# Kernel tuning notes

Measured on AMD Instinct MI355X. Metric: run time of the kernel, lower is better.

## Reference

```python
import jax, jax.numpy as jnp
import numpy as np

D = 768       # input embedding dim
H = 256       # hidden_dim
NH = 4        # num_heads
HD = H // NH  # head_dim = 64
M = 131072    # number of candidate LLM embeddings


def setup_inputs() -> dict:
    key = jax.random.key(0)
    ks = jax.random.split(key, 16)
    s = 0.02
    return {
        "user": jax.random.normal(ks[0], (D,), jnp.float32),
        "query": jax.random.normal(ks[1], (D,), jnp.float32),
        "llm": jax.random.normal(ks[2], (M, D), jnp.float32),
        # projection weights (torch Linear: y = x @ W.T + b)
        "Wu": jax.random.normal(ks[3], (H, D), jnp.float32) * s,
        "bu": jnp.zeros((H,), jnp.float32),
        "Wq": jax.random.normal(ks[4], (H, D), jnp.float32) * s,
        "bq": jnp.zeros((H,), jnp.float32),
        "Wl": jax.random.normal(ks[5], (H, D), jnp.float32) * s,
        "bl": jnp.zeros((H,), jnp.float32),
        # MultiheadAttention packed in-projection [3H, H] and bias [3H]
        "in_proj_w": jax.random.normal(ks[6], (3 * H, H), jnp.float32) * s,
        "in_proj_b": jnp.zeros((3 * H,), jnp.float32),
        "out_proj_w": jax.random.normal(ks[7], (H, H), jnp.float32) * s,
        "out_proj_b": jnp.zeros((H,), jnp.float32),
        # final scoring linear: [1, 2H]
        "Wo": jax.random.normal(ks[8], (1, 2 * H), jnp.float32) * s,
        "bo": jnp.zeros((1,), jnp.float32),
    }


def reference(user, query, llm, Wu, bu, Wq, bq, Wl, bl,
              in_proj_w, in_proj_b, out_proj_w, out_proj_b, Wo, bo):
    m = llm.shape[0]
    # input projections
    u = user @ Wu.T + bu            # [H]
    qv = query @ Wq.T + bq          # [H]
    l = llm @ Wl.T + bl             # [M, H]
    # context rows are identical for every candidate -> compute K/V once on [2, H]
    ctx = jnp.stack([u, qv], axis=0)                      # [2, H]
    Wq_a, Wk_a, Wv_a = jnp.split(in_proj_w, 3, axis=0)    # each [H, H]
    bq_a, bk_a, bv_a = jnp.split(in_proj_b, 3, axis=0)
    q = (l @ Wq_a.T + bq_a).reshape(m, NH, HD)            # [M, nh, hd] (seq_len=1)
    k = (ctx @ Wk_a.T + bk_a).reshape(2, NH, HD)          # [2, nh, hd]
    v = (ctx @ Wv_a.T + bv_a).reshape(2, NH, HD)
    scale = 1.0 / jnp.sqrt(jnp.asarray(HD, q.dtype))
    scores = jnp.einsum('mhd,khd->mhk', q, k) * scale     # [M, nh, 2]
    attn = jax.nn.softmax(scores, axis=-1)
    attended = jnp.einsum('mhk,khd->mhd', attn, v).reshape(m, H)
    attended = attended @ out_proj_w.T + out_proj_b       # [M, H]
    x = jnp.concatenate([attended, l], axis=-1)           # [M, 2H]
    # out = Sequential(ReLU, Dropout(eval=identity), Linear(2H, 1))
    logits = (jax.nn.relu(x) @ Wo.T + bo).squeeze(-1)     # [M]
    return logits
```

## Files before the change

kernel.cpp:

```cpp
#include <hip/hip_runtime.h>


typedef float f32x4 __attribute__((ext_vector_type(4)));
typedef __bf16 bf16x8 __attribute__((ext_vector_type(8)));

#define VMCNT(n) asm volatile("s_waitcnt vmcnt(" #n ")" ::: "memory")

__device__ __forceinline__ unsigned f2bf(float f) {
  unsigned u = __builtin_bit_cast(unsigned, f);
  u += 0x7fffu + ((u >> 16) & 1u);
  return u >> 16;
}

__device__ __forceinline__ void gl_lds16(const void* g, void* l) {
  __builtin_amdgcn_global_load_lds(
      (const __attribute__((address_space(1))) void*)g,
      (__attribute__((address_space(3))) void*)l, 16, 0, 0);
}

__global__ void prep_a(const float* __restrict__ user, const float* __restrict__ query,
                       const float* __restrict__ Wu, const float* __restrict__ bu,
                       const float* __restrict__ Wq, const float* __restrict__ bq,
                       float* __restrict__ wf) {
  const int og = threadIdx.x >> 5, ln = threadIdx.x & 31;
  const int o = blockIdx.x * 8 + og;
  const int isq = o >> 8, j = o & 255;
  const float* Wrow = (isq ? Wq : Wu) + (size_t)j * 768;
  const float* vec = isq ? query : user;
  float p = 0.f;
  #pragma unroll
  for (int i = 0; i < 24; ++i) { int d = ln * 24 + i; p = fmaf(Wrow[d], vec[d], p); }
  #pragma unroll
  for (int off = 16; off; off >>= 1) p += __shfl_xor(p, off);
  if (ln == 0) wf[o] = p + (isq ? bq[j] : bu[j]);
}

__global__ void prep_b(const float* __restrict__ ipw, const float* __restrict__ ipb,
                       float* __restrict__ wf) {
  const int og = threadIdx.x >> 5, ln = threadIdx.x & 31;
  const int o = blockIdx.x * 8 + og;
  const int kv = o >> 9, cc = (o >> 8) & 1, j = o & 255;
  const int row = 256 + kv * 256 + j;
  const float* Wrow = ipw + (size_t)row * 256;
  const float* ctx = wf + cc * 256;
  float p = 0.f;
  #pragma unroll
  for (int i = 0; i < 8; ++i) { int d = ln * 8 + i; p = fmaf(Wrow[d], ctx[d], p); }
  #pragma unroll
  for (int off = 16; off; off >>= 1) p += __shfl_xor(p, off);
  if (ln == 0) wf[512 + o] = p + ipb[row];
}

__global__ void prep_c(const float* __restrict__ ipw, const float* __restrict__ ipb,
                       const float* __restrict__ opw, const float* __restrict__ opb,
                       float* __restrict__ wf) {
  const int t = threadIdx.x, b = blockIdx.x;
  if (b < 4) {
    const int h = b;
    float acc = 0.f;
    for (int d = 0; d < 64; ++d) {
      float kd = wf[512 + h * 64 + d] - wf[768 + h * 64 + d];
      acc = fmaf(ipw[(size_t)(h * 64 + d) * 256 + t], kd, acc);
    }
    wf[1536 + h * 256 + t] = 0.125f * acc;
    if (t == 0) {
      float cs = 0.f;
      for (int d = 0; d < 64; ++d)
        cs = fmaf(ipb[h * 64 + d], wf[512 + h * 64 + d] - wf[768 + h * 64 + d], cs);
      wf[3840 + h] = 0.125f * cs;
    }
  } else {
    const float* oprow = opw + (size_t)t * 256;
    float bse = 0.f;
    for (int i = 0; i < 256; ++i) bse = fmaf(oprow[i], wf[1280 + i], bse);
    wf[2560 + t] = bse + opb[t];
    #pragma unroll
    for (int h = 0; h < 4; ++h) {
      float dl = 0.f;
      for (int d = 0; d < 64; ++d)
        dl = fmaf(oprow[h * 64 + d], wf[1024 + h * 64 + d] - wf[1280 + h * 64 + d], dl);
      wf[2816 + h * 256 + t] = dl;
    }
  }
}

__global__ void prep_w(const float* __restrict__ Wl, unsigned int* __restrict__ Bs4) {
  const int tid = blockIdx.x * 256 + threadIdx.x;
  const int lane = tid & 63;
  const int ntk = tid >> 6;
  const int kk = ntk >> 4, nt = ntk & 15;
  const int k = kk * 32 + (lane >> 4) * 8;
  const int j = nt * 16 + (lane & 15);
  const float* src = Wl + (size_t)j * 768 + k;
  uint4 pk;
  pk.x = f2bf(src[0]) | (f2bf(src[1]) << 16);
  pk.y = f2bf(src[2]) | (f2bf(src[3]) << 16);
  pk.z = f2bf(src[4]) | (f2bf(src[5]) << 16);
  pk.w = f2bf(src[6]) | (f2bf(src[7]) << 16);
  ((uint4*)Bs4)[tid] = pk;
}

__global__ __launch_bounds__(256, 3) void fused_main(
    const float* __restrict__ llm, const float* __restrict__ bl,
    const float* __restrict__ Wo, const float* __restrict__ bo,
    const float* __restrict__ wf, float* __restrict__ out) {

  __shared__ __align__(16) char smem[49152];
  __shared__ float csd_s[4];
  __shared__ float a_s[64][4];
  __shared__ float r2_s[64];
  __shared__ float p2_s[4][64];

  const int t = threadIdx.x;
  const int w = t >> 6, l = t & 63, g = l >> 4, c = l & 15;
  const int m0 = blockIdx.x * 64;
  const char* BsB = (const char*)(wf + 4096);

  auto stage = [&](int buf, int kk) {
    char* abase = smem + buf * 8192 + w * 1024;
    #pragma unroll
    for (int r = 0; r < 2; ++r) {
      const int chunk = r * 256 + w * 64 + l;
      const int row = chunk >> 3;
      const int cb = (chunk & 7) * 16;
      const int cl = cb ^ ((row & 7) << 4);
      const char* gp = (const char*)(llm + (size_t)(m0 + row) * 768 + kk * 32) + cl;
      gl_lds16(gp, abase + r * 4096);
    }
    char* bbase = smem + 16384 + buf * 16384 + w * 1024;
    const char* gb = BsB + (size_t)kk * 16384;
    #pragma unroll
    for (int r = 0; r < 4; ++r) {
      const int chunk = r * 256 + w * 64 + l;
      gl_lds16(gb + (size_t)chunk * 16, bbase + r * 4096);
    }
  };

  stage(0, 0);

  f32x4 acc[16] = {};
  const int row_l = w * 16 + c;
  const int sro = row_l * 128;
  const int sxor = (row_l & 7) << 4;

  for (int kk = 0; kk < 24; ++kk) {
    const int cur = kk & 1;
    if (kk < 23) { stage(cur ^ 1, kk + 1); VMCNT(6); }
    else         { VMCNT(0); }
    __builtin_amdgcn_s_barrier();

    const char* ab = smem + cur * 8192 + sro;
    const float4 fa = *(const float4*)(ab + ((g * 32) ^ sxor));
    const float4 fb = *(const float4*)(ab + ((g * 32 + 16) ^ sxor));
    uint4 pk;
    pk.x = f2bf(fa.x) | (f2bf(fa.y) << 16);
    pk.y = f2bf(fa.z) | (f2bf(fa.w) << 16);
    pk.z = f2bf(fb.x) | (f2bf(fb.y) << 16);
    pk.w = f2bf(fb.z) | (f2bf(fb.w) << 16);
    const bf16x8 afr = __builtin_bit_cast(bf16x8, pk);

    const char* bb = smem + 16384 + cur * 16384 + l * 16;
    #pragma unroll
    for (int nt = 0; nt < 16; ++nt) {
      const bf16x8 bfr = *(const bf16x8*)(bb + nt * 1024);
      acc[nt] = __builtin_amdgcn_mfma_f32_16x16x32_bf16(afr, bfr, acc[nt], 0, 0, 0);
    }
    __builtin_amdgcn_s_barrier();
  }

  float* wsd_s  = (float*)smem;
  float* delta_s = (float*)smem + 1024;
  float* base_s = (float*)smem + 2048;
  float* woa_s  = (float*)smem + 2304;
  float* wo2_s  = (float*)smem + 2560;
  float* bl_s   = (float*)smem + 2816;
  for (int i = t; i < 1024; i += 256) { wsd_s[i] = wf[1536 + i]; delta_s[i] = wf[2816 + i]; }
  base_s[t] = wf[2560 + t];
  woa_s[t] = Wo[t];
  wo2_s[t] = Wo[256 + t];
  bl_s[t] = bl[t];
  if (t < 4) csd_s[t] = wf[3840 + t];
  __syncthreads();

  float psd[4][4] = {};
  float pr2[4] = {};
  #pragma unroll
  for (int nt = 0; nt < 16; ++nt) {
    const int col = nt * 16 + c;
    const float w0 = wsd_s[col], w1 = wsd_s[256 + col], w2 = wsd_s[512 + col], w3 = wsd_s[768 + col];
    const float wo = wo2_s[col], bb2 = bl_s[col];
    #pragma unroll
    for (int j = 0; j < 4; ++j) {
      const float x = acc[nt][j] + bb2;
      psd[j][0] = fmaf(x, w0, psd[j][0]);
      psd[j][1] = fmaf(x, w1, psd[j][1]);
      psd[j][2] = fmaf(x, w2, psd[j][2]);
      psd[j][3] = fmaf(x, w3, psd[j][3]);
      pr2[j] = fmaf(fmaxf(x, 0.f), wo, pr2[j]);
    }
  }
  #pragma unroll
  for (int off = 8; off; off >>= 1) {
    #pragma unroll
    for (int j = 0; j < 4; ++j) {
      #pragma unroll
      for (int h = 0; h < 4; ++h) psd[j][h] += __shfl_xor(psd[j][h], off);
      pr2[j] += __shfl_xor(pr2[j], off);
    }
  }
  if (c == 0) {
    #pragma unroll
    for (int j = 0; j < 4; ++j) {
      const int r = w * 16 + g * 4 + j;
      #pragma unroll
      for (int h = 0; h < 4; ++h)
        a_s[r][h] = 1.f / (1.f + __expf(-(psd[j][h] + csd_s[h])));
      r2_s[r] = pr2[j];
    }
  }
  __syncthreads();

  {
    const int r = t & 63, q = t >> 6;
    const float a0 = a_s[r][0], a1 = a_s[r][1], a2 = a_s[r][2], a3 = a_s[r][3];
    float p = 0.f;
    const int j0 = q * 64;
    #pragma unroll 4
    for (int j = j0; j < j0 + 64; ++j) {
      float att = base_s[j];
      att = fmaf(a0, delta_s[j], att);
      att = fmaf(a1, delta_s[256 + j], att);
      att = fmaf(a2, delta_s[512 + j], att);
      att = fmaf(a3, delta_s[768 + j], att);
      p = fmaf(fmaxf(att, 0.f), woa_s[j], p);
    }
    p2_s[q][r] = p;
  }
  __syncthreads();
  if (t < 64)
    out[m0 + t] = p2_s[0][t] + p2_s[1][t] + p2_s[2][t] + p2_s[3][t] + r2_s[t] + bo[0];
}

extern "C" void kernel_launch(void* const* d_in, const int* in_sizes, int n_in,
                              void* d_out, int out_size, void* d_ws, size_t ws_size,
                              hipStream_t stream) {
  const float* user  = (const float*)d_in[0];
  const float* query = (const float*)d_in[1];
  const float* llm   = (const float*)d_in[2];
  const float* Wu    = (const float*)d_in[3];
  const float* bu    = (const float*)d_in[4];
  const float* Wq    = (const float*)d_in[5];
  const float* bq    = (const float*)d_in[6];
  const float* Wl    = (const float*)d_in[7];
  const float* bl    = (const float*)d_in[8];
  const float* ipw   = (const float*)d_in[9];
  const float* ipb   = (const float*)d_in[10];
  const float* opw   = (const float*)d_in[11];
  const float* opb   = (const float*)d_in[12];
  const float* Wo    = (const float*)d_in[13];
  const float* bo    = (const float*)d_in[14];
  float* out = (float*)d_out;
  float* wf = (float*)d_ws;
  unsigned int* Bs4 = (unsigned int*)(wf + 4096);

  prep_a<<<64, 256, 0, stream>>>(user, query, Wu, bu, Wq, bq, wf);
  prep_w<<<96, 256, 0, stream>>>(Wl, Bs4);
  prep_b<<<128, 256, 0, stream>>>(ipw, ipb, wf);
  prep_c<<<5, 256, 0, stream>>>(ipw, ipb, opw, opb, wf);
  fused_main<<<131072 / 64, 256, 0, stream>>>(llm, bl, Wo, bo, wf, out);
}
```

Baseline: 167.8 us.

## Keep Wl B-fragments in registers and split waves over output columns

The main GEMM loop stops staging the pre-packed bf16 Wl tiles through LDS. Each wave now owns 64 output columns and loads its B fragments straight from global memory into double-buffered registers. The A tile (the fp32 llm rows) moves to a triple-buffered LDS ring with prefetch two steps ahead, and one barrier per step replaces two. This halves shared-memory use and removes the B LDS traffic, which may allow higher occupancy. The cost is a cross-wave partial-sum reduction through LDS in the epilogue, and each wave now converts four A fragments to bf16 per step instead of one, repeating that conversion across waves.

Result: no change. 171.1 us (+2.0%).

```diff
diff --git a/kernel.cpp b/kernel.cpp
--- a/kernel.cpp
+++ b/kernel.cpp
@@ -105,7 +105,7 @@
     const float* __restrict__ Wo, const float* __restrict__ bo,
     const float* __restrict__ wf, float* __restrict__ out) {
 
-  __shared__ __align__(16) char smem[49152];
+  __shared__ __align__(16) char smem[24576];
   __shared__ float csd_s[4];
   __shared__ float a_s[64][4];
   __shared__ float r2_s[64];
@@ -116,8 +116,8 @@
   const int m0 = blockIdx.x * 64;
   const char* BsB = (const char*)(wf + 4096);
 
-  auto stage = [&](int buf, int kk) {
-    char* abase = smem + buf * 8192 + w * 1024;
+  auto stageA = [&](int slot, int kk) {
+    char* abase = smem + slot * 8192 + w * 1024;
     #pragma unroll
     for (int r = 0; r < 2; ++r) {
       const int chunk = r * 256 + w * 64 + l;
@@ -127,53 +127,71 @@
       const char* gp = (const char*)(llm + (size_t)(m0 + row) * 768 + kk * 32) + cl;
       gl_lds16(gp, abase + r * 4096);
     }
-    char* bbase = smem + 16384 + buf * 16384 + w * 1024;
-    const char* gb = BsB + (size_t)kk * 16384;
-    #pragma unroll
-    for (int r = 0; r < 4; ++r) {
-      const int chunk = r * 256 + w * 64 + l;
-      gl_lds16(gb + (size_t)chunk * 16, bbase + r * 4096);
-    }
   };
 
-  stage(0, 0);
-
-  f32x4 acc[16] = {};
-  const int row_l = w * 16 + c;
-  const int sro = row_l * 128;
-  const int sxor = (row_l & 7) << 4;
-
-  for (int kk = 0; kk < 24; ++kk) {
-    const int cur = kk & 1;
-    if (kk < 23) { stage(cur ^ 1, kk + 1); VMCNT(6); }
-    else         { VMCNT(0); }
+  uint4 b0[4], b1[4];
+
+  stageA(0, 0);
+  {
+    const char* gb = BsB + (size_t)l * 16;
+    #pragma unroll
+    for (int cf = 0; cf < 4; ++cf)
+      b0[cf] = *(const uint4*)(gb + (w * 4 + cf) * 1024);
+  }
+  stageA(1, 1);
+
+  f32x4 acc[4][4] = {};
+  const int sx = (c & 7) << 4;
+
+  auto step = [&](int kk, int slot, int nslot2, uint4* use, uint4* fill) {
+    if (kk < 23) { VMCNT(2); } else { VMCNT(0); }
     __builtin_amdgcn_s_barrier();
-
-    const char* ab = smem + cur * 8192 + sro;
-    const float4 fa = *(const float4*)(ab + ((g * 32) ^ sxor));
-    const float4 fb = *(const float4*)(ab + ((g * 32 + 16) ^ sxor));
-    uint4 pk;
-    pk.x = f2bf(fa.x) | (f2bf(fa.y) << 16);
-    pk.y = f2bf(fa.z) | (f2bf(fa.w) << 16);
-    pk.z = f2bf(fb.x) | (f2bf(fb.y) << 16);
-    pk.w = f2bf(fb.z) | (f2bf(fb.w) << 16);
-    const bf16x8 afr = __builtin_bit_cast(bf16x8, pk);
-
-    const char* bb = smem + 16384 + cur * 16384 + l * 16;
-    #pragma unroll
-    for (int nt = 0; nt < 16; ++nt) {
-      const bf16x8 bfr = *(const bf16x8*)(bb + nt * 1024);
-      acc[nt] = __builtin_amdgcn_mfma_f32_16x16x32_bf16(afr, bfr, acc[nt], 0, 0, 0);
-    }
-    __builtin_amdgcn_s_barrier();
-  }
-
-  float* wsd_s  = (float*)smem;
-  float* delta_s = (float*)smem + 1024;
-  float* base_s = (float*)smem + 2048;
-  float* woa_s  = (float*)smem + 2304;
-  float* wo2_s  = (float*)smem + 2560;
-  float* bl_s   = (float*)smem + 2816;
+    __builtin_amdgcn_sched_barrier(0);
+    if (kk < 23) {
+      const char* gb = BsB + (size_t)(kk + 1) * 16384 + (size_t)l * 16;
+      #pragma unroll
+      for (int cf = 0; cf < 4; ++cf)
+        fill[cf] = *(const uint4*)(gb + (w * 4 + cf) * 1024);
+    }
+    if (kk < 22) stageA(nslot2, kk + 2);
+    const char* ab = smem + slot * 8192;
+    #pragma unroll
+    for (int rf = 0; rf < 4; ++rf) {
+      const char* rp = ab + (rf * 16 + c) * 128;
+      const float4 fa = *(const float4*)(rp + ((g * 32) ^ sx));
+      const float4 fb = *(const float4*)(rp + ((g * 32 + 16) ^ sx));
+      uint4 pk;
+      pk.x = f2bf(fa.x) | (f2bf(fa.y) << 16);
+      pk.y = f2bf(fa.z) | (f2bf(fa.w) << 16);
+      pk.z = f2bf(fb.x) | (f2bf(fb.y) << 16);
+      pk.w = f2bf(fb.z) | (f2bf(fb.w) << 16);
+      const bf16x8 afr = __builtin_bit_cast(bf16x8, pk);
+      #pragma unroll
+      for (int cf = 0; cf < 4; ++cf)
+        acc[rf][cf] = __builtin_amdgcn_mfma_f32_16x16x32_bf16(
+            afr, __builtin_bit_cast(bf16x8, use[cf]), acc[rf][cf], 0, 0, 0);
+    }
+  };
+
+  for (int kk = 0; kk < 24; kk += 2) {
+    const int s0 = kk % 3;
+    const int s1 = (s0 + 1 == 3) ? 0 : s0 + 1;
+    const int s2 = (s1 + 1 == 3) ? 0 : s1 + 1;
+    step(kk,     s0, s2, b0, b1);
+    step(kk + 1, s1, s0, b1, b0);
+  }
+
+  __syncthreads();
+
+  float* smf = (float*)smem;
+  float* wsd_s  = smf;
+  float* delta_s = smf + 1024;
+  float* base_s = smf + 2048;
+  float* woa_s  = smf + 2304;
+  float* wo2_s  = smf + 2560;
+  float* bl_s   = smf + 2816;
+  float* psd_p  = smf + 3072;
+  float* pr2_p  = smf + 4096;
   for (int i = t; i < 1024; i += 256) { wsd_s[i] = wf[1536 + i]; delta_s[i] = wf[2816 + i]; }
   base_s[t] = wf[2560 + t];
   woa_s[t] = Wo[t];
@@ -182,41 +200,59 @@
   if (t < 4) csd_s[t] = wf[3840 + t];
   __syncthreads();
 
-  float psd[4][4] = {};
-  float pr2[4] = {};
-  #pragma unroll
-  for (int nt = 0; nt < 16; ++nt) {
-    const int col = nt * 16 + c;
-    const float w0 = wsd_s[col], w1 = wsd_s[256 + col], w2 = wsd_s[512 + col], w3 = wsd_s[768 + col];
-    const float wo = wo2_s[col], bb2 = bl_s[col];
-    #pragma unroll
-    for (int j = 0; j < 4; ++j) {
-      const float x = acc[nt][j] + bb2;
-      psd[j][0] = fmaf(x, w0, psd[j][0]);
-      psd[j][1] = fmaf(x, w1, psd[j][1]);
-      psd[j][2] = fmaf(x, w2, psd[j][2]);
-      psd[j][3] = fmaf(x, w3, psd[j][3]);
-      pr2[j] = fmaf(fmaxf(x, 0.f), wo, pr2[j]);
-    }
-  }
-  #pragma unroll
-  for (int off = 8; off; off >>= 1) {
-    #pragma unroll
-    for (int j = 0; j < 4; ++j) {
-      #pragma unroll
-      for (int h = 0; h < 4; ++h) psd[j][h] += __shfl_xor(psd[j][h], off);
-      pr2[j] += __shfl_xor(pr2[j], off);
-    }
-  }
-  if (c == 0) {
-    #pragma unroll
-    for (int j = 0; j < 4; ++j) {
-      const int r = w * 16 + g * 4 + j;
-      #pragma unroll
-      for (int h = 0; h < 4; ++h)
-        a_s[r][h] = 1.f / (1.f + __expf(-(psd[j][h] + csd_s[h])));
-      r2_s[r] = pr2[j];
-    }
+  #pragma unroll
+  for (int rf = 0; rf < 4; ++rf) {
+    float psd[4][4] = {};
+    float pr2[4] = {};
+    #pragma unroll
+    for (int cf = 0; cf < 4; ++cf) {
+      const int col = w * 64 + cf * 16 + c;
+      const float w0 = wsd_s[col], w1 = wsd_s[256 + col],
+                  w2 = wsd_s[512 + col], w3 = wsd_s[768 + col];
+      const float wo = wo2_s[col], bb2 = bl_s[col];
+      #pragma unroll
+      for (int j = 0; j < 4; ++j) {
+        const float x = acc[rf][cf][j] + bb2;
+        psd[j][0] = fmaf(x, w0, psd[j][0]);
+        psd[j][1] = fmaf(x, w1, psd[j][1]);
+        psd[j][2] = fmaf(x, w2, psd[j][2]);
+        psd[j][3] = fmaf(x, w3, psd[j][3]);
+        pr2[j] = fmaf(fmaxf(x, 0.f), wo, pr2[j]);
+      }
+    }
+    #pragma unroll
+    for (int off = 8; off; off >>= 1) {
+      #pragma unroll
+      for (int j = 0; j < 4; ++j) {
+        #pragma unroll
+        for (int h = 0; h < 4; ++h) psd[j][h] += __shfl_xor(psd[j][h], off);
+        pr2[j] += __shfl_xor(pr2[j], off);
+      }
+    }
+    if (c == 0) {
+      #pragma unroll
+      for (int j = 0; j < 4; ++j) {
+        const int row = rf * 16 + g * 4 + j;
+        #pragma unroll
+        for (int h = 0; h < 4; ++h) psd_p[w * 256 + row * 4 + h] = psd[j][h];
+        pr2_p[w * 64 + row] = pr2[j];
+      }
+    }
+  }
+  __syncthreads();
+
+  if (t < 64) {
+    #pragma unroll
+    for (int h = 0; h < 4; ++h) {
+      float sd = csd_s[h];
+      #pragma unroll
+      for (int ww = 0; ww < 4; ++ww) sd += psd_p[ww * 256 + t * 4 + h];
+      a_s[t][h] = 1.f / (1.f + __expf(-sd));
+    }
+    float rr = 0.f;
+    #pragma unroll
+    for (int ww = 0; ww < 4; ++ww) rr += pr2_p[ww * 64 + t];
+    r2_s[t] = rr;
   }
   __syncthreads();
 
```
